# Kernel optimization log

Hardware: AMD Instinct MI355X
Metric: run time of the kernel (lower is better)

Reference implementation:

```python
import jax, jax.numpy as jnp
import numpy as np

N, E = 100000, 1600000
IN_C, HID, OUT_C = 128, 128, 64
HOPS, L = 2, 3
EPS = 1e-5


def setup_inputs() -> dict:
    key = jax.random.key(0)
    ks = jax.random.split(key, 16)
    x = jax.random.normal(ks[0], (N, IN_C), jnp.float32)
    edge_index = jax.random.randint(ks[1], (2, E), 0, N, dtype=jnp.int32).astype(jnp.int64)
    CAT = HID * (HOPS + 1)  # 384
    def lin(k, fan_in, fan_out, nstack):
        return jax.random.normal(k, (nstack, fan_in, fan_out), jnp.float32) / np.sqrt(fan_in)
    return {
        "x": x,
        "edge_index": edge_index,
        "W0": lin(ks[2], IN_C, HID, HOPS + 1),
        "b0": jnp.zeros((HOPS + 1, HID), jnp.float32),
        "W1": lin(ks[3], CAT, HID, HOPS + 1),
        "b1": jnp.zeros((HOPS + 1, HID), jnp.float32),
        "W2": lin(ks[4], CAT, OUT_C, HOPS + 1),
        "b2": jnp.zeros((HOPS + 1, OUT_C), jnp.float32),
        "bn0_g": jnp.ones((CAT,), jnp.float32),
        "bn0_b": jnp.zeros((CAT,), jnp.float32),
        "bn1_g": jnp.ones((CAT,), jnp.float32),
        "bn1_b": jnp.zeros((CAT,), jnp.float32),
        "fpW": jax.random.normal(ks[5], (OUT_C * (HOPS + 1), OUT_C), jnp.float32) / np.sqrt(OUT_C * (HOPS + 1)),
        "fpb": jnp.zeros((OUT_C,), jnp.float32),
    }


def reference(x, edge_index, W0, b0, W1, b1, W2, b2,
              bn0_g, bn0_b, bn1_g, bn1_b, fpW, fpb):
    row, col = edge_index[0], edge_index[1]
    # gcn_norm with add_self_loops=False, unit edge weights:
    # deg = scatter_add(1, col); w_e = deg^-1/2[row] * deg^-1/2[col]
    deg = jnp.zeros((N,), x.dtype).at[col].add(1.0)
    dinv = jnp.where(deg > 0, jax.lax.rsqrt(jnp.maximum(deg, 1.0)), 0.0)
    ew = dinv[row] * dinv[col]

    def spmm(h):
        # adj_t = SparseTensor(row=col, col=row, value=ew): out[col] += ew * h[row]
        return jax.ops.segment_sum(ew[:, None] * h[row], col, num_segments=N)

    def mixhop(h, W, b):
        outs = []
        for j in range(HOPS + 1):
            hj = h @ W[j] + b[j]          # lins[j](h)
            for _ in range(j):
                hj = spmm(hj)             # A^j applied j times
            outs.append(hj)
        return jnp.concatenate(outs, axis=1)

    def bn(h, g, bb):
        # BatchNorm1d in training mode: batch stats, biased variance
        mu = h.mean(axis=0)
        var = h.var(axis=0)
        return g * (h - mu) * jax.lax.rsqrt(var + EPS) + bb

    h = jax.nn.relu(bn(mixhop(x, W0, b0), bn0_g, bn0_b))   # dropout: identity (eval)
    h = jax.nn.relu(bn(mixhop(h, W1, b1), bn1_g, bn1_b))
    h = mixhop(h, W2, b2)
    return h @ fpW + fpb
```

## Files before the change

kernel.cpp:

```cpp
#include <hip/hip_runtime.h>
#include <cstdint>
#include <cstddef>

#define IN_C 128
#define HIDc 128
#define OUTc 64

using bf8 = __attribute__((ext_vector_type(8))) __bf16;
using f4  = __attribute__((ext_vector_type(4))) float;

__device__ __forceinline__ unsigned short f2bf(float f) {
    unsigned int u = __float_as_uint(f);
    unsigned int r = (u + 0x7FFFu + ((u >> 16) & 1u)) >> 16;
    return (unsigned short)r;
}
__device__ __forceinline__ float bf2f(unsigned short h) {
    return __uint_as_float(((unsigned int)h) << 16);
}

__device__ __forceinline__ void gload16(const unsigned short* g, unsigned short* l) {
    __builtin_amdgcn_global_load_lds(
        (const __attribute__((address_space(1))) unsigned int*)g,
        (__attribute__((address_space(3))) unsigned int*)l, 16, 0, 0);
}

__global__ void k_detect(const long long* ei, int n_nodes, int* flag) {
    int t = threadIdx.x;
    long long v = ei[t];
    int ok = (v >= 0 && v < (long long)n_nodes) ? 1 : 0;
    unsigned long long m = __ballot(ok);
    if (t == 0) *flag = (m == ~0ull) ? 1 : 0;
}

__global__ void k_cvt_hist(const void* ei, int twoE, int E, const int* flag,
                           int* __restrict__ out, int* __restrict__ deg, int n) {
    int i = blockIdx.x * blockDim.x + threadIdx.x;
    if (i >= twoE) return;
    int v = (*flag) ? (int)((const long long*)ei)[i] : ((const int*)ei)[i];
    out[i] = v;
    if (i >= E && (unsigned)v < (unsigned)n) atomicAdd(&deg[v], 1);
}

__global__ void k_dinv(const int* __restrict__ deg, float* __restrict__ dinv, int n) {
    int i = blockIdx.x * blockDim.x + threadIdx.x;
    if (i < n) dinv[i] = (deg[i] > 0) ? rsqrtf((float)deg[i]) : 0.0f;
}

__global__ void k_alloc(const int* __restrict__ deg, int* __restrict__ base,
                        int* __restrict__ cursor, int* __restrict__ counter, int n) {
    int i = blockIdx.x * blockDim.x + threadIdx.x;
    int lane = threadIdx.x & 63;
    int val = (i < n) ? deg[i] : 0;
    int scan = val;
    #pragma unroll
    for (int off = 1; off < 64; off <<= 1) {
        int t = __shfl_up(scan, off);
        if (lane >= off) scan += t;
    }
    int excl = scan - val;
    int total = __shfl(scan, 63);
    int wb = 0;
    if (lane == 0) wb = atomicAdd(counter, total);
    wb = __shfl(wb, 0);
    if (i < n) { base[i] = wb + excl; cursor[i] = wb + excl; }
}

__global__ void k_scatter(const int* __restrict__ eint, int E,
                          const float* __restrict__ dinv, int n,
                          int* __restrict__ cursor, int2* __restrict__ ew) {
    int e = blockIdx.x * blockDim.x + threadIdx.x;
    if (e >= E) return;
    int r = eint[e];
    int c = eint[E + e];
    if ((unsigned)r >= (unsigned)n || (unsigned)c >= (unsigned)n) return;
    int p = atomicAdd(&cursor[c], 1);
    int2 v; v.x = r; v.y = __float_as_int(dinv[r] * dinv[c]);
    ew[p] = v;
}

__global__ void k_wprep(const float* __restrict__ W, unsigned short* __restrict__ Wt,
                        int K, int N) {
    int j = blockIdx.y;
    int idx = blockIdx.x * 256 + threadIdx.x;
    if (idx >= K * N) return;
    int k = idx / N, nn = idx - k * N;
    Wt[(size_t)j * N * K + (size_t)nn * K + k] = f2bf(W[(size_t)j * K * N + idx]);
}

__global__ void k_cast4(const float* __restrict__ x, unsigned short* __restrict__ y, int n4) {
    int i = blockIdx.x * 256 + threadIdx.x;
    if (i >= n4) return;
    float4 v = ((const float4*)x)[i];
    ushort4 o;
    o.x = f2bf(v.x); o.y = f2bf(v.y); o.z = f2bf(v.z); o.w = f2bf(v.w);
    ((ushort4*)y)[i] = o;
}

template<int TILEN, bool BFOUT>
__global__ __launch_bounds__(256) void k_gemm(
    const unsigned short* __restrict__ A0, const unsigned short* __restrict__ A1,
    const unsigned short* __restrict__ A2, int W, int M, int K,
    const unsigned short* __restrict__ Bt,
    const float* __restrict__ bias,
    unsigned short* __restrict__ C0, unsigned short* __restrict__ C1,
    unsigned short* __restrict__ C2, float* __restrict__ Cf)
{
    constexpr int TM = 4;
    constexpr int TN = TILEN / 32;
    __shared__ __align__(16) unsigned short As[128 * 32];
    __shared__ __align__(16) unsigned short Bs[TILEN * 32];

    int t = threadIdx.x;
    int wave = t >> 6, lane = t & 63;
    int m16 = lane & 15, q = lane >> 4;
    int j = blockIdx.y;
    int row0 = blockIdx.x * 128;
    int wr = (wave & 1) * 64;
    int wc = (wave >> 1) * (TILEN / 2);

    int lr = lane >> 2, lch = lane & 3;
    int ra0 = (wave * 2 + 0) * 16 + lr;
    int ra1 = (wave * 2 + 1) * 16 + lr;
    int ga0 = row0 + ra0; if (ga0 >= M) ga0 = M - 1;
    int ga1 = row0 + ra1; if (ga1 >= M) ga1 = M - 1;
    size_t boff0 = (size_t)(j * TILEN + ra0) * K;
    size_t boff1 = (size_t)(j * TILEN + ra1) * K;
    size_t boffS = (size_t)(j * TILEN + wave * 16 + lr) * K;

    f4 acc[TM][TN];
    #pragma unroll
    for (int i = 0; i < TM; i++)
        #pragma unroll
        for (int jj = 0; jj < TN; jj++) acc[i][jj] = (f4){0.f, 0.f, 0.f, 0.f};

    for (int kk = 0; kk < K; kk += 32) {
        int pi = kk / W;
        const unsigned short* Ap = (pi == 0) ? A0 : ((pi == 1) ? A1 : A2);
        int kl = kk - pi * W;

        __syncthreads();
        gload16(&Ap[(size_t)ga0 * W + kl + lch * 8], &As[(wave * 2 + 0) * 512]);
        gload16(&Ap[(size_t)ga1 * W + kl + lch * 8], &As[(wave * 2 + 1) * 512]);
        if (TILEN == 128) {
            gload16(&Bt[boff0 + kk + lch * 8], &Bs[(wave * 2 + 0) * 512]);
            gload16(&Bt[boff1 + kk + lch * 8], &Bs[(wave * 2 + 1) * 512]);
        } else {
            gload16(&Bt[boffS + kk + lch * 8], &Bs[wave * 512]);
        }
        __syncthreads();

        bf8 af[TM], bfr[TN];
        #pragma unroll
        for (int tm = 0; tm < TM; tm++)
            af[tm] = *(const bf8*)&As[(wr + tm * 16 + m16) * 32 + q * 8];
        #pragma unroll
        for (int tn = 0; tn < TN; tn++)
            bfr[tn] = *(const bf8*)&Bs[(wc + tn * 16 + m16) * 32 + q * 8];
        #pragma unroll
        for (int tm = 0; tm < TM; tm++)
            #pragma unroll
            for (int tn = 0; tn < TN; tn++)
                acc[tm][tn] = __builtin_amdgcn_mfma_f32_16x16x32_bf16(
                    af[tm], bfr[tn], acc[tm][tn], 0, 0, 0);
    }

    unsigned short* Cj = (j == 0) ? C0 : ((j == 1) ? C1 : C2);
    #pragma unroll
    for (int tn = 0; tn < TN; tn++) {
        int col = wc + tn * 16 + m16;
        float bi = bias[j * TILEN + col];
        #pragma unroll
        for (int tm = 0; tm < TM; tm++) {
            #pragma unroll
            for (int r = 0; r < 4; r++) {
                int row = row0 + wr + tm * 16 + q * 4 + r;
                if (row >= M) continue;
                float v = acc[tm][tn][r] + bi;
                if (BFOUT) Cj[(size_t)row * TILEN + col] = f2bf(v);
                else       Cf[(size_t)row * TILEN + col] = v;
            }
        }
    }
}

template<int V, bool DUAL>
__global__ __launch_bounds__(256) void k_spmm(
    const unsigned short* __restrict__ S1, const unsigned short* __restrict__ S2,
    unsigned short* __restrict__ D1, unsigned short* __restrict__ D2, int width,
    const int* __restrict__ base, const int* __restrict__ deg,
    const int2* __restrict__ ew, int n)
{
    int node = blockIdx.x * 4 + threadIdx.y;
    if (node >= n) return;
    int tx = threadIdx.x;
    float a1[V], a2[V];
    #pragma unroll
    for (int v = 0; v < V; v++) { a1[v] = 0.f; if (DUAL) a2[v] = 0.f; }
    int b = base[node], end = b + deg[node];
    const unsigned short* P1 = S1 + tx * V;
    const unsigned short* P2 = DUAL ? (S2 + tx * V) : nullptr;
    constexpr int UN = 8;
    int e = b;
    for (; e + UN <= end; e += UN) {
        int2 ev[UN];
        #pragma unroll
        for (int u = 0; u < UN; u++) ev[u] = ew[e + u];
        unsigned int g1[UN], g2[UN];
        #pragma unroll
        for (int u = 0; u < UN; u++) {
            if (V == 2) g1[u] = *(const unsigned int*)(P1 + (size_t)ev[u].x * width);
            else        g1[u] = P1[(size_t)ev[u].x * width];
            if (DUAL) {
                if (V == 2) g2[u] = *(const unsigned int*)(P2 + (size_t)ev[u].x * width);
                else        g2[u] = P2[(size_t)ev[u].x * width];
            }
        }
        #pragma unroll
        for (int u = 0; u < UN; u++) {
            float we = __int_as_float(ev[u].y);
            if (V == 2) {
                a1[0] += we * bf2f((unsigned short)(g1[u] & 0xffff));
                a1[1] += we * bf2f((unsigned short)(g1[u] >> 16));
                if (DUAL) {
                    a2[0] += we * bf2f((unsigned short)(g2[u] & 0xffff));
                    a2[1] += we * bf2f((unsigned short)(g2[u] >> 16));
                }
            } else {
                a1[0] += we * bf2f((unsigned short)g1[u]);
                if (DUAL) a2[0] += we * bf2f((unsigned short)g2[u]);
            }
        }
    }
    for (; e < end; ++e) {
        int2 ev = ew[e];
        float we = __int_as_float(ev.y);
        if (V == 2) {
            unsigned int u1 = *(const unsigned int*)(P1 + (size_t)ev.x * width);
            a1[0] += we * bf2f((unsigned short)(u1 & 0xffff));
            a1[1] += we * bf2f((unsigned short)(u1 >> 16));
            if (DUAL) {
                unsigned int u2 = *(const unsigned int*)(P2 + (size_t)ev.x * width);
                a2[0] += we * bf2f((unsigned short)(u2 & 0xffff));
                a2[1] += we * bf2f((unsigned short)(u2 >> 16));
            }
        } else {
            a1[0] += we * bf2f(P1[(size_t)ev.x * width]);
            if (DUAL) a2[0] += we * bf2f(P2[(size_t)ev.x * width]);
        }
    }
    size_t o = (size_t)node * width + tx * V;
    if (V == 2) {
        ushort2 o1; o1.x = f2bf(a1[0]); o1.y = f2bf(a1[1]);
        *(ushort2*)&D1[o] = o1;
        if (DUAL) { ushort2 o2; o2.x = f2bf(a2[0]); o2.y = f2bf(a2[1]);
                    *(ushort2*)&D2[o] = o2; }
    } else {
        D1[o] = f2bf(a1[0]);
        if (DUAL) D2[o] = f2bf(a2[0]);
    }
}

__global__ void k_bnstats(const unsigned short* __restrict__ p0,
                          const unsigned short* __restrict__ p1,
                          const unsigned short* __restrict__ p2,
                          float* __restrict__ sums, float* __restrict__ sumsq, int n)
{
    int c = threadIdx.x;
    int cc = c & 127;
    int pi = c >> 7;
    const unsigned short* src = (pi == 0) ? p0 : ((pi == 1) ? p1 : p2);
    float s = 0.f, s2 = 0.f;
    for (int r = blockIdx.x; r < n; r += gridDim.x) {
        float v = bf2f(src[(size_t)r * 128 + cc]);
        s += v; s2 += v * v;
    }
    atomicAdd(&sums[c], s);
    atomicAdd(&sumsq[c], s2);
}

__global__ void k_bnfin(const float* __restrict__ sums, const float* __restrict__ sumsq,
                        const float* __restrict__ g, const float* __restrict__ bb,
                        float* __restrict__ scale, float* __restrict__ shift,
                        int cat, float invn)
{
    int c = threadIdx.x;
    if (c >= cat) return;
    float mu  = sums[c] * invn;
    float var = sumsq[c] * invn - mu * mu;
    float sc  = g[c] * rsqrtf(var + 1e-5f);
    scale[c] = sc;
    shift[c] = bb[c] - mu * sc;
}

__global__ void k_bnapply(unsigned short* __restrict__ p0, unsigned short* __restrict__ p1,
                          unsigned short* __restrict__ p2,
                          const float* __restrict__ scale, const float* __restrict__ shift,
                          int n)
{
    int c = threadIdx.x;
    int cc = c & 127;
    int pi = c >> 7;
    unsigned short* src = (pi == 0) ? p0 : ((pi == 1) ? p1 : p2);
    float sc = scale[c], sh = shift[c];
    for (int r = blockIdx.x; r < n; r += gridDim.x) {
        size_t idx = (size_t)r * 128 + cc;
        float v = bf2f(src[idx]) * sc + sh;
        src[idx] = f2bf(fmaxf(v, 0.0f));
    }
}

__global__ void k_diag(float* out, float val, int n) {
    int i = blockIdx.x * blockDim.x + threadIdx.x;
    if (i < n) out[i] = val;
}

extern "C" void kernel_launch(void* const* d_in, const int* in_sizes, int n_in,
                              void* d_out, int out_size, void* d_ws, size_t ws_size,
                              hipStream_t stream)
{
    const float* x    = (const float*)d_in[0];
    const void*  ei   = d_in[1];
    const float* W0   = (const float*)d_in[2];
    const float* b0   = (const float*)d_in[3];
    const float* W1   = (const float*)d_in[4];
    const float* b1   = (const float*)d_in[5];
    const float* W2   = (const float*)d_in[6];
    const float* b2   = (const float*)d_in[7];
    const float* bn0g = (const float*)d_in[8];
    const float* bn0b = (const float*)d_in[9];
    const float* bn1g = (const float*)d_in[10];
    const float* bn1b = (const float*)d_in[11];
    const float* fpW  = (const float*)d_in[12];
    const float* fpb  = (const float*)d_in[13];
    float* out = (float*)d_out;

    const int N    = in_sizes[0] / IN_C;
    const int twoE = in_sizes[1];
    const int E    = twoE / 2;

    char* p = (char*)d_ws;
    auto alloc = [&](size_t bytes) -> char* {
        char* r = p; p += (bytes + 255) & ~(size_t)255; return r;
    };
    unsigned short* U[6];
    for (int i = 0; i < 6; i++) U[i] = (unsigned short*)alloc((size_t)N * 128 * 2);
    unsigned short* Wt0 = (unsigned short*)alloc((size_t)3 * 128 * 128 * 2);
    unsigned short* Wt1 = (unsigned short*)alloc((size_t)3 * 384 * 128 * 2);
    unsigned short* Wt2 = (unsigned short*)alloc((size_t)3 * 384 * 64 * 2);
    unsigned short* WtF = (unsigned short*)alloc((size_t)192 * 64 * 2);
    float* dinv  = (float*)alloc((size_t)N * 4);
    int2*  ew    = (int2*)alloc((size_t)E * 8);
    float* sums  = (float*)alloc(2 * 384 * 4);
    float* sumsq = sums + 384;
    float* scale = (float*)alloc(384 * 4);
    float* shift = (float*)alloc(384 * 4);
    int* deg     = (int*)alloc((size_t)N * 4);
    int* base    = (int*)alloc((size_t)N * 4);
    int* cursor  = (int*)alloc((size_t)N * 4);
    int* eint    = (int*)alloc((size_t)twoE * 4);
    int* counter = (int*)alloc(4);
    int* flag    = (int*)alloc(4);

    size_t required = (size_t)(p - (char*)d_ws);
    if (required > ws_size) {
        k_diag<<<(out_size + 255) / 256, 256, 0, stream>>>(
            out, (float)(ws_size >> 20), out_size);
        return;
    }

    const int T = 256;
    dim3 spmm_blk(64, 4);
    int  spmm_grid = (N + 3) / 4;
    int  gx = (N + 127) / 128;

    k_wprep<<<dim3((128 * 128 + 255) / 256, 3), T, 0, stream>>>(W0, Wt0, 128, 128);
    k_wprep<<<dim3((384 * 128 + 255) / 256, 3), T, 0, stream>>>(W1, Wt1, 384, 128);
    k_wprep<<<dim3((384 * 64  + 255) / 256, 3), T, 0, stream>>>(W2, Wt2, 384, 64);
    k_wprep<<<dim3((192 * 64  + 255) / 256, 1), T, 0, stream>>>(fpW, WtF, 192, 64);
    unsigned short* Xb = U[3];
    k_cast4<<<((N * 128 / 4) + 255) / 256, T, 0, stream>>>(x, Xb, N * 128 / 4);

    hipMemsetAsync(deg, 0, (size_t)N * 4, stream);
    hipMemsetAsync(counter, 0, 4, stream);
    k_detect<<<1, 64, 0, stream>>>((const long long*)ei, N, flag);
    k_cvt_hist<<<(twoE + T - 1) / T, T, 0, stream>>>(ei, twoE, E, flag, eint, deg, N);
    k_dinv<<<(N + T - 1) / T, T, 0, stream>>>(deg, dinv, N);
    k_alloc<<<(N + T - 1) / T, T, 0, stream>>>(deg, base, cursor, counter, N);
    k_scatter<<<(E + T - 1) / T, T, 0, stream>>>(eint, E, dinv, N, cursor, ew);

    k_gemm<128, true><<<dim3(gx, 3), T, 0, stream>>>(Xb, Xb, Xb, 128, N, 128,
        Wt0, b0, U[0], U[1], U[2], nullptr);
    k_spmm<2, true ><<<spmm_grid, spmm_blk, 0, stream>>>(U[1], U[2], U[4], U[5], 128,
                                                         base, deg, ew, N);
    k_spmm<2, false><<<spmm_grid, spmm_blk, 0, stream>>>(U[5], nullptr, U[3], nullptr, 128,
                                                         base, deg, ew, N);
    hipMemsetAsync(sums, 0, 2 * 384 * 4, stream);
    k_bnstats<<<2048, 384, 0, stream>>>(U[0], U[4], U[3], sums, sumsq, N);
    k_bnfin<<<1, 384, 0, stream>>>(sums, sumsq, bn0g, bn0b, scale, shift, 384, 1.0f / N);
    k_bnapply<<<2048, 384, 0, stream>>>(U[0], U[4], U[3], scale, shift, N);

    k_gemm<128, true><<<dim3(gx, 3), T, 0, stream>>>(U[0], U[4], U[3], 128, N, 384,
        Wt1, b1, U[1], U[2], U[5], nullptr);
    k_spmm<2, true ><<<spmm_grid, spmm_blk, 0, stream>>>(U[2], U[5], U[0], U[4], 128,
                                                         base, deg, ew, N);
    k_spmm<2, false><<<spmm_grid, spmm_blk, 0, stream>>>(U[4], nullptr, U[3], nullptr, 128,
                                                         base, deg, ew, N);
    hipMemsetAsync(sums, 0, 2 * 384 * 4, stream);
    k_bnstats<<<2048, 384, 0, stream>>>(U[1], U[0], U[3], sums, sumsq, N);
    k_bnfin<<<1, 384, 0, stream>>>(sums, sumsq, bn1g, bn1b, scale, shift, 384, 1.0f / N);
    k_bnapply<<<2048, 384, 0, stream>>>(U[1], U[0], U[3], scale, shift, N);

    unsigned short* V2a = U[2];
    unsigned short* V2b = U[2] + (size_t)N * 64;
    unsigned short* V4a = U[4];
    unsigned short* V4b = U[4] + (size_t)N * 64;
    unsigned short* V5a = U[5];
    unsigned short* V5b = U[5] + (size_t)N * 64;
    k_gemm<64, true><<<dim3(gx, 3), T, 0, stream>>>(U[1], U[0], U[3], 128, N, 384,
        Wt2, b2, V2a, V2b, V4a, nullptr);
    k_spmm<1, true ><<<spmm_grid, spmm_blk, 0, stream>>>(V2b, V4a, V4b, V5a, 64,
                                                         base, deg, ew, N);
    k_spmm<1, false><<<spmm_grid, spmm_blk, 0, stream>>>(V5a, nullptr, V5b, nullptr, 64,
                                                         base, deg, ew, N);

    k_gemm<64, false><<<dim3(gx, 1), T, 0, stream>>>(V2a, V4b, V5b, 64, N, 192,
        WtF, fpb, nullptr, nullptr, nullptr, out);
}
```

Baseline: 1.314 ms.

## Interleave hop-1/hop-2 GEMM outputs and stage GEMM epilogue through LDS

The GEMM now writes its outputs with per-output leading dimensions, so the hop-1 and hop-2 projections are stored interleaved in one row of width 2*C. The dual SpMM becomes a single kernel where each half-wave gathers one half of that combined row, so each gathered neighbour row is one contiguous segment instead of two separate reads. The GEMM epilogue also stages results in a 16 KB shared buffer and writes them back as coalesced 16-byte stores instead of scattered 2-byte stores. The cost is extra shared memory and barriers in the GEMM, which may lower occupancy.

```diff
diff --git a/kernel.cpp b/kernel.cpp
--- a/kernel.cpp
+++ b/kernel.cpp
@@ -102,13 +102,16 @@
     const unsigned short* __restrict__ A2, int W, int M, int K,
     const unsigned short* __restrict__ Bt,
     const float* __restrict__ bias,
-    unsigned short* __restrict__ C0, unsigned short* __restrict__ C1,
-    unsigned short* __restrict__ C2, float* __restrict__ Cf)
+    unsigned short* __restrict__ C0, int ldc0,
+    unsigned short* __restrict__ C1, int ldc1,
+    unsigned short* __restrict__ C2, int ldc2,
+    float* __restrict__ Cf, int ldcf)
 {
     constexpr int TM = 4;
     constexpr int TN = TILEN / 32;
     __shared__ __align__(16) unsigned short As[128 * 32];
     __shared__ __align__(16) unsigned short Bs[TILEN * 32];
+    __shared__ __align__(16) unsigned char  Cs[16384];
 
     int t = threadIdx.x;
     int wave = t >> 6, lane = t & 63;
@@ -164,56 +167,142 @@
                     af[tm], bfr[tn], acc[tm][tn], 0, 0, 0);
     }
 
-    unsigned short* Cj = (j == 0) ? C0 : ((j == 1) ? C1 : C2);
+    constexpr int EB  = BFOUT ? 2 : 4;
+    constexpr int RB  = TILEN * EB;
+    constexpr int CPR = RB / 16;
+    constexpr int PT  = 64 * CPR / 256;
+    char* Cb;
+    long  ldb;
+    if (BFOUT) {
+        unsigned short* Cj = (j == 0) ? C0 : ((j == 1) ? C1 : C2);
+        int lj = (j == 0) ? ldc0 : ((j == 1) ? ldc1 : ldc2);
+        Cb = (char*)Cj; ldb = (long)lj * 2;
+    } else {
+        Cb = (char*)Cf; ldb = (long)ldcf * 4;
+    }
     #pragma unroll
-    for (int tn = 0; tn < TN; tn++) {
-        int col = wc + tn * 16 + m16;
-        float bi = bias[j * TILEN + col];
-        #pragma unroll
-        for (int tm = 0; tm < TM; tm++) {
+    for (int half = 0; half < 2; half++) {
+        __syncthreads();
+        if ((wave & 1) == half) {
             #pragma unroll
-            for (int r = 0; r < 4; r++) {
-                int row = row0 + wr + tm * 16 + q * 4 + r;
-                if (row >= M) continue;
-                float v = acc[tm][tn][r] + bi;
-                if (BFOUT) Cj[(size_t)row * TILEN + col] = f2bf(v);
-                else       Cf[(size_t)row * TILEN + col] = v;
+            for (int tn = 0; tn < TN; tn++) {
+                int col = wc + tn * 16 + m16;
+                float bi = bias[j * TILEN + col];
+                #pragma unroll
+                for (int tm = 0; tm < TM; tm++) {
+                    #pragma unroll
+                    for (int r = 0; r < 4; r++) {
+                        int lrow = tm * 16 + q * 4 + r;
+                        float v = acc[tm][tn][r] + bi;
+                        if (BFOUT) ((unsigned short*)Cs)[lrow * TILEN + col] = f2bf(v);
+                        else       ((float*)Cs)[lrow * TILEN + col] = v;
+                    }
+                }
             }
         }
-    }
-}
-
-template<int V, bool DUAL>
-__global__ __launch_bounds__(256) void k_spmm(
-    const unsigned short* __restrict__ S1, const unsigned short* __restrict__ S2,
-    unsigned short* __restrict__ D1, unsigned short* __restrict__ D2, int width,
+        __syncthreads();
+        #pragma unroll
+        for (int i = 0; i < PT; i++) {
+            int idx  = i * 256 + t;
+            int lrow = idx / CPR;
+            int c16  = idx - lrow * CPR;
+            int grow = row0 + half * 64 + lrow;
+            if (grow < M)
+                *(uint4*)(Cb + (size_t)grow * ldb + c16 * 16) = ((const uint4*)Cs)[idx];
+        }
+    }
+}
+
+template<int PW>
+__global__ __launch_bounds__(256) void k_spmm2i(
+    const unsigned short* __restrict__ S,
+    unsigned short* __restrict__ D1, unsigned short* __restrict__ D2,
     const int* __restrict__ base, const int* __restrict__ deg,
     const int2* __restrict__ ew, int n)
 {
     int node = blockIdx.x * 4 + threadIdx.y;
     if (node >= n) return;
-    int tx = threadIdx.x;
-    float a1[V], a2[V];
+    int lane = threadIdx.x;
+    constexpr int CV = PW / 32;
+    int half = lane >> 5, lx = lane & 31;
+    const unsigned short* Sp = S + half * PW + lx * CV;
+    float acc[CV];
     #pragma unroll
-    for (int v = 0; v < V; v++) { a1[v] = 0.f; if (DUAL) a2[v] = 0.f; }
+    for (int v = 0; v < CV; v++) acc[v] = 0.f;
     int b = base[node], end = b + deg[node];
-    const unsigned short* P1 = S1 + tx * V;
-    const unsigned short* P2 = DUAL ? (S2 + tx * V) : nullptr;
     constexpr int UN = 8;
     int e = b;
     for (; e + UN <= end; e += UN) {
         int2 ev[UN];
         #pragma unroll
         for (int u = 0; u < UN; u++) ev[u] = ew[e + u];
-        unsigned int g1[UN], g2[UN];
+        ushort4 g4[UN]; ushort2 g2[UN];
+        #pragma unroll
+        for (int u = 0; u < UN; u++) {
+            if (CV == 4) g4[u] = *(const ushort4*)(Sp + (size_t)ev[u].x * (2 * PW));
+            else         g2[u] = *(const ushort2*)(Sp + (size_t)ev[u].x * (2 * PW));
+        }
+        #pragma unroll
+        for (int u = 0; u < UN; u++) {
+            float we = __int_as_float(ev[u].y);
+            if (CV == 4) {
+                acc[0] += we * bf2f(g4[u].x); acc[1] += we * bf2f(g4[u].y);
+                acc[2] += we * bf2f(g4[u].z); acc[3] += we * bf2f(g4[u].w);
+            } else {
+                acc[0] += we * bf2f(g2[u].x); acc[1] += we * bf2f(g2[u].y);
+            }
+        }
+    }
+    for (; e < end; ++e) {
+        int2 ev = ew[e];
+        float we = __int_as_float(ev.y);
+        if (CV == 4) {
+            ushort4 g = *(const ushort4*)(Sp + (size_t)ev.x * (2 * PW));
+            acc[0] += we * bf2f(g.x); acc[1] += we * bf2f(g.y);
+            acc[2] += we * bf2f(g.z); acc[3] += we * bf2f(g.w);
+        } else {
+            ushort2 g = *(const ushort2*)(Sp + (size_t)ev.x * (2 * PW));
+            acc[0] += we * bf2f(g.x); acc[1] += we * bf2f(g.y);
+        }
+    }
+    unsigned short* D = half ? D2 : D1;
+    size_t o = (size_t)node * PW + lx * CV;
+    if (CV == 4) {
+        ushort4 ov;
+        ov.x = f2bf(acc[0]); ov.y = f2bf(acc[1]);
+        ov.z = f2bf(acc[2]); ov.w = f2bf(acc[3]);
+        *(ushort4*)&D[o] = ov;
+    } else {
+        ushort2 ov; ov.x = f2bf(acc[0]); ov.y = f2bf(acc[1]);
+        *(ushort2*)&D[o] = ov;
+    }
+}
+
+template<int V>
+__global__ __launch_bounds__(256) void k_spmm(
+    const unsigned short* __restrict__ S1, unsigned short* __restrict__ D1, int width,
+    const int* __restrict__ base, const int* __restrict__ deg,
+    const int2* __restrict__ ew, int n)
+{
+    int node = blockIdx.x * 4 + threadIdx.y;
+    if (node >= n) return;
+    int tx = threadIdx.x;
+    float a1[V];
+    #pragma unroll
+    for (int v = 0; v < V; v++) a1[v] = 0.f;
+    int b = base[node], end = b + deg[node];
+    const unsigned short* P1 = S1 + tx * V;
+    constexpr int UN = 8;
+    int e = b;
+    for (; e + UN <= end; e += UN) {
+        int2 ev[UN];
+        #pragma unroll
+        for (int u = 0; u < UN; u++) ev[u] = ew[e + u];
+        unsigned int g1[UN];
         #pragma unroll
         for (int u = 0; u < UN; u++) {
             if (V == 2) g1[u] = *(const unsigned int*)(P1 + (size_t)ev[u].x * width);
             else        g1[u] = P1[(size_t)ev[u].x * width];
-            if (DUAL) {
-                if (V == 2) g2[u] = *(const unsigned int*)(P2 + (size_t)ev[u].x * width);
-                else        g2[u] = P2[(size_t)ev[u].x * width];
-            }
         }
         #pragma unroll
         for (int u = 0; u < UN; u++) {
@@ -221,13 +310,8 @@
             if (V == 2) {
                 a1[0] += we * bf2f((unsigned short)(g1[u] & 0xffff));
                 a1[1] += we * bf2f((unsigned short)(g1[u] >> 16));
-                if (DUAL) {
-                    a2[0] += we * bf2f((unsigned short)(g2[u] & 0xffff));
-                    a2[1] += we * bf2f((unsigned short)(g2[u] >> 16));
-                }
             } else {
                 a1[0] += we * bf2f((unsigned short)g1[u]);
-                if (DUAL) a2[0] += we * bf2f((unsigned short)g2[u]);
             }
         }
     }
@@ -238,25 +322,16 @@
             unsigned int u1 = *(const unsigned int*)(P1 + (size_t)ev.x * width);
             a1[0] += we * bf2f((unsigned short)(u1 & 0xffff));
             a1[1] += we * bf2f((unsigned short)(u1 >> 16));
-            if (DUAL) {
-                unsigned int u2 = *(const unsigned int*)(P2 + (size_t)ev.x * width);
-                a2[0] += we * bf2f((unsigned short)(u2 & 0xffff));
-                a2[1] += we * bf2f((unsigned short)(u2 >> 16));
-            }
         } else {
             a1[0] += we * bf2f(P1[(size_t)ev.x * width]);
-            if (DUAL) a2[0] += we * bf2f(P2[(size_t)ev.x * width]);
         }
     }
     size_t o = (size_t)node * width + tx * V;
     if (V == 2) {
         ushort2 o1; o1.x = f2bf(a1[0]); o1.y = f2bf(a1[1]);
         *(ushort2*)&D1[o] = o1;
-        if (DUAL) { ushort2 o2; o2.x = f2bf(a2[0]); o2.y = f2bf(a2[1]);
-                    *(ushort2*)&D2[o] = o2; }
     } else {
         D1[o] = f2bf(a1[0]);
-        if (DUAL) D2[o] = f2bf(a2[0]);
     }
 }
 
@@ -342,8 +417,12 @@
     auto alloc = [&](size_t bytes) -> char* {
         char* r = p; p += (bytes + 255) & ~(size_t)255; return r;
     };
-    unsigned short* U[6];
-    for (int i = 0; i < 6; i++) U[i] = (unsigned short*)alloc((size_t)N * 128 * 2);
+    unsigned short* u0 = (unsigned short*)alloc((size_t)6 * N * 128 * 2);
+    unsigned short* u1 = u0 + (size_t)1 * N * 128;
+    unsigned short* u2 = u0 + (size_t)2 * N * 128;
+    unsigned short* u3 = u0 + (size_t)3 * N * 128;
+    unsigned short* u4 = u0 + (size_t)4 * N * 128;
+    unsigned short* u5 = u0 + (size_t)5 * N * 128;
     unsigned short* Wt0 = (unsigned short*)alloc((size_t)3 * 128 * 128 * 2);
     unsigned short* Wt1 = (unsigned short*)alloc((size_t)3 * 384 * 128 * 2);
     unsigned short* Wt2 = (unsigned short*)alloc((size_t)3 * 384 * 64 * 2);
@@ -377,7 +456,7 @@
     k_wprep<<<dim3((384 * 128 + 255) / 256, 3), T, 0, stream>>>(W1, Wt1, 384, 128);
     k_wprep<<<dim3((384 * 64  + 255) / 256, 3), T, 0, stream>>>(W2, Wt2, 384, 64);
     k_wprep<<<dim3((192 * 64  + 255) / 256, 1), T, 0, stream>>>(fpW, WtF, 192, 64);
-    unsigned short* Xb = U[3];
+    unsigned short* Xb = u3;
     k_cast4<<<((N * 128 / 4) + 255) / 256, T, 0, stream>>>(x, Xb, N * 128 / 4);
 
     hipMemsetAsync(deg, 0, (size_t)N * 4, stream);
@@ -389,40 +468,30 @@
     k_scatter<<<(E + T - 1) / T, T, 0, stream>>>(eint, E, dinv, N, cursor, ew);
 
     k_gemm<128, true><<<dim3(gx, 3), T, 0, stream>>>(Xb, Xb, Xb, 128, N, 128,
-        Wt0, b0, U[0], U[1], U[2], nullptr);
-    k_spmm<2, true ><<<spmm_grid, spmm_blk, 0, stream>>>(U[1], U[2], U[4], U[5], 128,
-                                                         base, deg, ew, N);
-    k_spmm<2, false><<<spmm_grid, spmm_blk, 0, stream>>>(U[5], nullptr, U[3], nullptr, 128,
-                                                         base, deg, ew, N);
+        Wt0, b0, u0, 128, u1, 256, u1 + 128, 256, nullptr, 0);
+    k_spmm2i<128><<<spmm_grid, spmm_blk, 0, stream>>>(u1, u4, u5, base, deg, ew, N);
+    k_spmm<2><<<spmm_grid, spmm_blk, 0, stream>>>(u5, u3, 128, base, deg, ew, N);
     hipMemsetAsync(sums, 0, 2 * 384 * 4, stream);
-    k_bnstats<<<2048, 384, 0, stream>>>(U[0], U[4], U[3], sums, sumsq, N);
+    k_bnstats<<<2048, 384, 0, stream>>>(u0, u4, u3, sums, sumsq, N);
     k_bnfin<<<1, 384, 0, stream>>>(sums, sumsq, bn0g, bn0b, scale, shift, 384, 1.0f / N);
-    k_bnapply<<<2048, 384, 0, stream>>>(U[0], U[4], U[3], scale, shift, N);
-
-    k_gemm<128, true><<<dim3(gx, 3), T, 0, stream>>>(U[0], U[4], U[3], 128, N, 384,
-        Wt1, b1, U[1], U[2], U[5], nullptr);
-    k_spmm<2, true ><<<spmm_grid, spmm_blk, 0, stream>>>(U[2], U[5], U[0], U[4], 128,
-                                                         base, deg, ew, N);
-    k_spmm<2, false><<<spmm_grid, spmm_blk, 0, stream>>>(U[4], nullptr, U[3], nullptr, 128,
-                                                         base, deg, ew, N);
+    k_bnapply<<<2048, 384, 0, stream>>>(u0, u4, u3, scale, shift, N);
+
+    k_gemm<128, true><<<dim3(gx, 3), T, 0, stream>>>(u0, u4, u3, 128, N, 384,
+        Wt1, b1, u5, 128, u1, 256, u1 + 128, 256, nullptr, 0);
+    k_spmm2i<128><<<spmm_grid, spmm_blk, 0, stream>>>(u1, u0, u4, base, deg, ew, N);
+    k_spmm<2><<<spmm_grid, spmm_blk, 0, stream>>>(u4, u3, 128, base, deg, ew, N);
     hipMemsetAsync(sums, 0, 2 * 384 * 4, stream);
-    k_bnstats<<<2048, 384, 0, stream>>>(U[1], U[0], U[3], sums, sumsq, N);
+    k_bnstats<<<2048, 384, 0, stream>>>(u5, u0, u3, sums, sumsq, N);
     k_bnfin<<<1, 384, 0, stream>>>(sums, sumsq, bn1g, bn1b, scale, shift, 384, 1.0f / N);
-    k_bnapply<<<2048, 384, 0, stream>>>(U[1], U[0], U[3], scale, shift, N);
-
-    unsigned short* V2a = U[2];
-    unsigned short* V2b = U[2] + (size_t)N * 64;
-    unsigned short* V4a = U[4];
-    unsigned short* V4b = U[4] + (size_t)N * 64;
-    unsigned short* V5a = U[5];
-    unsigned short* V5b = U[5] + (size_t)N * 64;
-    k_gemm<64, true><<<dim3(gx, 3), T, 0, stream>>>(U[1], U[0], U[3], 128, N, 384,
-        Wt2, b2, V2a, V2b, V4a, nullptr);
-    k_spmm<1, true ><<<spmm_grid, spmm_blk, 0, stream>>>(V2b, V4a, V4b, V5a, 64,
-                                                         base, deg, ew, N);
-    k_spmm<1, false><<<spmm_grid, spmm_blk, 0, stream>>>(V5a, nullptr, V5b, nullptr, 64,
-                                                         base, deg, ew, N);
-
-    k_gemm<64, false><<<dim3(gx, 1), T, 0, stream>>>(V2a, V4b, V5b, 64, N, 192,
-        WtF, fpb, nullptr, nullptr, nullptr, out);
-}
+    k_bnapply<<<2048, 384, 0, stream>>>(u5, u0, u3, scale, shift, N);
+
+    k_gemm<64, true><<<dim3(gx, 3), T, 0, stream>>>(u5, u0, u3, 128, N, 384,
+        Wt2, b2, u1, 64, u2, 128, u2 + 64, 128, nullptr, 0);
+    k_spmm2i<64><<<spmm_grid, spmm_blk, 0, stream>>>(u2, u4, u4 + (size_t)N * 64,
+                                                     base, deg, ew, N);
+    k_spmm<1><<<spmm_grid, spmm_blk, 0, stream>>>(u4 + (size_t)N * 64, u5, 64,
+                                                  base, deg, ew, N);
+
+    k_gemm<64, false><<<dim3(gx, 1), T, 0, stream>>>(u1, u4, u5, 64, N, 192,
+        WtF, fpb, nullptr, 0, nullptr, 0, nullptr, 0, out, 64);
+}
```

After: 1.235 ms. 1.06x faster.
